# Optimization experiments

Hardware: AMD Instinct MI355X
Metric: run time of the kernel (lower is better)

Reference implementation:

```python
import jax, jax.numpy as jnp
import numpy as np

N_NODES = 100000
N_EDGES = 1600000
D_IN = 128
CH = [128, 128]
N_GRAPHS = 256


def _glorot(key, shape):
    lim = float(np.sqrt(6.0 / (shape[0] + shape[1])))
    return jax.random.uniform(key, shape, jnp.float32, -lim, lim)


def setup_inputs() -> dict:
    key = jax.random.key(0)
    ks = jax.random.split(key, 12)
    x = jax.random.normal(ks[0], (N_NODES, D_IN), jnp.float32)
    edge_index = jax.random.randint(ks[1], (2, N_EDGES), 0, N_NODES, jnp.int64)
    batch = jnp.sort(jax.random.randint(ks[2], (N_NODES,), 0, N_GRAPHS, jnp.int64))
    W1 = _glorot(ks[3], (D_IN, CH[0]))
    b1 = jnp.zeros((CH[0],), jnp.float32)
    W2 = _glorot(ks[4], (CH[0], CH[1]))
    b2 = jnp.zeros((CH[1],), jnp.float32)
    Wm1 = _glorot(ks[5], (CH[1], 500)); bm1 = jnp.zeros((500,), jnp.float32)
    Wm2 = _glorot(ks[6], (500, 100));   bm2 = jnp.zeros((100,), jnp.float32)
    Wm3 = _glorot(ks[7], (100, 1));     bm3 = jnp.zeros((1,), jnp.float32)
    return {"x": x, "edge_index": edge_index, "batch": batch,
            "W1": W1, "b1": b1, "W2": W2, "b2": b2,
            "Wm1": Wm1, "bm1": bm1, "Wm2": Wm2, "bm2": bm2,
            "Wm3": Wm3, "bm3": bm3}


def gcn_conv(x, W, b, src, dst, n_nodes):
    # GCNConv with add_self_loops=True, symmetric normalization.
    h = x @ W  # [N, C]
    deg = jnp.zeros((n_nodes,), h.dtype).at[dst].add(1.0) + 1.0  # +1 self loop
    dinv = jax.lax.rsqrt(deg)  # deg >= 1
    norm = dinv[src] * dinv[dst]  # [E]
    agg = jnp.zeros_like(h).at[dst].add(h[src] * norm[:, None])
    agg = agg + h * (dinv * dinv)[:, None]  # self-loop term, norm = dinv[i]^2
    return agg + b


def global_mean_pool(x, batch, n_graphs):
    s = jax.ops.segment_sum(x, batch, num_segments=n_graphs)
    cnt = jax.ops.segment_sum(jnp.ones((x.shape[0],), x.dtype), batch, num_segments=n_graphs)
    return s / jnp.maximum(cnt, 1.0)[:, None]


def reference(x, edge_index, batch, W1, b1, W2, b2, Wm1, bm1, Wm2, bm2, Wm3, bm3):
    src, dst = edge_index[0], edge_index[1]
    h = jax.nn.relu(gcn_conv(x, W1, b1, src, dst, N_NODES))
    h = jax.nn.relu(gcn_conv(h, W2, b2, src, dst, N_NODES))
    g = global_mean_pool(h, batch, N_GRAPHS)  # [G, CH1]
    g = jax.nn.relu(g @ Wm1 + bm1)
    g = jax.nn.relu(g @ Wm2 + bm2)
    return g @ Wm3 + bm3  # [G, 1]
```

## Files before the change

### kernel.cpp

```cpp
#include <hip/hip_runtime.h>

#define CDIM 128
#define NGRAPH 256
#define BSH 7
#define BCAP 4096
#define NBLK 256

typedef unsigned short bf16_t;
typedef __attribute__((ext_vector_type(8))) short bf16x8;
typedef __attribute__((ext_vector_type(4))) float f32x4;

__device__ __forceinline__ float bflo(unsigned u) { return __uint_as_float(u << 16); }
__device__ __forceinline__ float bfhi(unsigned u) { return __uint_as_float(u & 0xffff0000u); }
__device__ __forceinline__ unsigned short f2bf(float f) {
  unsigned u = __float_as_uint(f);
  u += 0x7fffu + ((u >> 16) & 1u);
  return (unsigned short)(u >> 16);
}

__global__ __launch_bounds__(1024) void k_phist(const int* __restrict__ dst,
    int* __restrict__ phist, const float* __restrict__ W1,
    const float* __restrict__ W2, bf16_t* __restrict__ Wtg1,
    bf16_t* __restrict__ Wtg2, float* __restrict__ gb, bf16_t* __restrict__ tz1,
    bf16_t* __restrict__ tz2, int N, int E, int NB) {
  __shared__ int hist[1024];
  int t = blockIdx.x, tid = threadIdx.x;
  int gidx = t * 1024 + tid;
  if (gidx < 16384) {
    int n = gidx >> 7, k = gidx & 127;
    Wtg1[n * 128 + k] = f2bf(W1[k * 128 + n]);
    Wtg2[n * 128 + k] = f2bf(W2[k * 128 + n]);
  }
  if (gidx < NGRAPH * CDIM) gb[gidx] = 0.f;
  if (gidx < 64) {
    ((unsigned*)(tz1 + (size_t)N * CDIM))[gidx] = 0u;
    ((unsigned*)(tz2 + (size_t)N * CDIM))[gidx] = 0u;
  }
  for (int i = tid; i < NB; i += 1024) hist[i] = 0;
  __syncthreads();
  int tile = (E + NBLK - 1) / NBLK;
  int lo = t * tile;
  int hi = lo + tile; if (hi > E) hi = E;
  for (int i = lo + tid; i < hi; i += 1024) atomicAdd(&hist[dst[i] >> BSH], 1);
  __syncthreads();
  for (int i = tid; i < NB; i += 1024) phist[i * NBLK + t] = hist[i];
}

__global__ __launch_bounds__(256) void k_bscan(int* __restrict__ phist,
    int* __restrict__ btot) {
  __shared__ int wsum[4];
  int b = blockIdx.x;
  int tid = threadIdx.x, lane = tid & 63, wave = tid >> 6;
  int orig = phist[b * NBLK + tid];
  int v = orig;
#pragma unroll
  for (int ofs = 1; ofs < 64; ofs <<= 1) {
    int u = __shfl_up(v, ofs, 64);
    if (lane >= ofs) v += u;
  }
  if (lane == 63) wsum[wave] = v;
  __syncthreads();
  int add = 0;
#pragma unroll
  for (int w = 0; w < 3; w++) if (w < wave) add += wsum[w];
  int incl = v + add;
  phist[b * NBLK + tid] = incl - orig;
  if (tid == 255) btot[b] = incl;
}

__global__ __launch_bounds__(1024) void k_pscatter(const int* __restrict__ src,
    const int* __restrict__ dst, const int* __restrict__ phist,
    const int* __restrict__ btot, unsigned* __restrict__ tmp, int E, int NB) {
  __shared__ int cur[1024];
  __shared__ int sh[1024];
  int t = blockIdx.x, tid = threadIdx.x;
  int v = (tid < NB) ? btot[tid] : 0;
  sh[tid] = v;
  __syncthreads();
  for (int ofs = 1; ofs < 1024; ofs <<= 1) {
    int u = (tid >= ofs) ? sh[tid - ofs] : 0;
    __syncthreads();
    sh[tid] += u;
    __syncthreads();
  }
  if (tid < NB) cur[tid] = (sh[tid] - v) + phist[tid * NBLK + t];
  __syncthreads();
  int tile = (E + NBLK - 1) / NBLK;
  int lo = t * tile;
  int hi = lo + tile; if (hi > E) hi = E;
  for (int i = lo + tid; i < hi; i += 1024) {
    int d = dst[i];
    int p = atomicAdd(&cur[d >> BSH], 1);
    tmp[p] = (unsigned)src[i] | ((unsigned)(d & 127) << 20);
  }
}

__global__ __launch_bounds__(256) void k_csort2(const unsigned* __restrict__ tmp,
    const int* __restrict__ btot, int* __restrict__ rowptr, float* __restrict__ dinv,
    int* __restrict__ col, int N, int NB, int E) {
  __shared__ int hist[128];
  __shared__ int sc[128];
  __shared__ int lcur[128];
  __shared__ int red[256];
  __shared__ unsigned buf[BCAP];
  int b = blockIdx.x;
  int n0 = b << BSH;
  int tid = threadIdx.x;
  int part = 0;
  for (int j = tid; j < b; j += 256) part += btot[j];
  red[tid] = part;
  __syncthreads();
  for (int ofs = 128; ofs > 0; ofs >>= 1) {
    if (tid < ofs) red[tid] += red[tid + ofs];
    __syncthreads();
  }
  int base = red[0];
  int cnt = btot[b];
  if (tid < 128) hist[tid] = 0;
  __syncthreads();
  for (int i = tid; i < cnt; i += 256) atomicAdd(&hist[(tmp[base + i] >> 20) & 127], 1);
  __syncthreads();
  if (tid < 128) sc[tid] = hist[tid];
  __syncthreads();
  for (int ofs = 1; ofs < 128; ofs <<= 1) {
    int v = (tid < 128 && tid >= ofs) ? sc[tid - ofs] : 0;
    __syncthreads();
    if (tid < 128) sc[tid] += v;
    __syncthreads();
  }
  if (tid < 128) {
    int excl = sc[tid] - hist[tid];
    lcur[tid] = excl;
    int node = n0 + tid;
    if (node < N) {
      rowptr[node] = base + excl;
      dinv[node] = rsqrtf((float)hist[tid] + 1.0f);
    }
  }
  if (b == 0 && tid == 0) rowptr[N] = E;
  __syncthreads();
  if (cnt <= BCAP) {
    for (int i = tid; i < cnt; i += 256) {
      unsigned pk = tmp[base + i];
      int p = atomicAdd(&lcur[(pk >> 20) & 127], 1);
      buf[p] = pk & 0xFFFFFu;
    }
    __syncthreads();
    for (int i = tid; i < cnt; i += 256) col[base + i] = (int)buf[i];
  } else {
    for (int i = tid; i < cnt; i += 256) {
      unsigned pk = tmp[base + i];
      int p = atomicAdd(&lcur[(pk >> 20) & 127], 1);
      col[base + p] = (int)(pk & 0xFFFFFu);
    }
  }
}

#define WSTRIDE 136
template <int BF16IN>
__global__ __launch_bounds__(256) void k_gemm(const void* __restrict__ Ap,
    const bf16_t* __restrict__ Wtg, const float* __restrict__ dscale,
    bf16_t* __restrict__ Co, int M) {
  __shared__ bf16_t Wt[128 * WSTRIDE];
  int tid = threadIdx.x;
  for (int c2 = tid; c2 < 2048; c2 += 256) {
    int n = c2 >> 4;
    int k8 = (c2 & 15) << 3;
    *(uint4*)&Wt[n * WSTRIDE + k8] = *(const uint4*)&Wtg[n * 128 + k8];
  }
  __syncthreads();

  int wave = tid >> 6;
  int lane = tid & 63;
  int m = lane & 15;
  int q = lane >> 4;
  int nstrips = (M + 63) >> 6;

  for (int s = blockIdx.x; s < nstrips; s += gridDim.x) {
    int rowA = s * 64 + wave * 16 + m;
    if (rowA > M - 1) rowA = M - 1;
    bf16x8 a[4];
#pragma unroll
    for (int c = 0; c < 4; c++) {
      if (BF16IN) {
        a[c] = *(const bf16x8*)((const bf16_t*)Ap + (size_t)rowA * CDIM + c * 32 + q * 8);
      } else {
        const float* ap = (const float*)Ap + (size_t)rowA * CDIM + c * 32 + q * 8;
        float4 f0 = *(const float4*)ap;
        float4 f1 = *(const float4*)(ap + 4);
        union { bf16x8 v; unsigned short u[8]; } ua;
        ua.u[0] = f2bf(f0.x); ua.u[1] = f2bf(f0.y); ua.u[2] = f2bf(f0.z); ua.u[3] = f2bf(f0.w);
        ua.u[4] = f2bf(f1.x); ua.u[5] = f2bf(f1.y); ua.u[6] = f2bf(f1.z); ua.u[7] = f2bf(f1.w);
        a[c] = ua.v;
      }
    }
    float sc[4];
#pragma unroll
    for (int r = 0; r < 4; r++) {
      int row = s * 64 + wave * 16 + q * 4 + r;
      sc[r] = (row < M) ? dscale[row] : 0.f;
    }
#pragma unroll
    for (int t = 0; t < 8; t++) {
      f32x4 acc = {0.f, 0.f, 0.f, 0.f};
#pragma unroll
      for (int c = 0; c < 4; c++) {
        bf16x8 bv = *(const bf16x8*)&Wt[(t * 16 + m) * WSTRIDE + c * 32 + q * 8];
        acc = __builtin_amdgcn_mfma_f32_16x16x32_bf16(a[c], bv, acc, 0, 0, 0);
      }
#pragma unroll
      for (int r = 0; r < 4; r++) {
        int row = s * 64 + wave * 16 + q * 4 + r;
        if (row < M) Co[(size_t)row * CDIM + t * 16 + m] = f2bf(acc[r] * sc[r]);
      }
    }
  }
}

#define GISS(S, V, JJ) \
  { _Pragma("unroll") for (int u = 0; u < 8; u++) \
      S[u] = __builtin_amdgcn_readlane(sL, (JJ) + u); \
    _Pragma("unroll") for (int u = 0; u < 8; u++) \
      V[u] = tp[(size_t)S[u] * 64 + lane]; }
#define GCON(V) \
  { _Pragma("unroll") for (int u = 0; u < 8; u++) { \
      a0 += bflo(V[u]); a1 += bfhi(V[u]); } }
#define GBLOCK(CNT) \
  { int nb = ((CNT) + 7) >> 3; \
    GISS(sA, vA, 0); \
    int b_ = 1; \
    for (; b_ + 1 < nb; b_ += 2) { \
      GISS(sB, vB, b_ * 8);       GCON(vA); \
      GISS(sA, vA, (b_ + 1) * 8); GCON(vB); \
    } \
    if (b_ < nb) { GISS(sB, vB, b_ * 8); GCON(vA); GCON(vB); } \
    else { GCON(vA); } }

__global__ __launch_bounds__(1024) void k_aggg(const bf16_t* __restrict__ t,
    const int* __restrict__ rowptr, const int* __restrict__ col,
    const float* __restrict__ dinv, const float* __restrict__ bias,
    const bf16_t* __restrict__ Wtg, bf16_t* __restrict__ to, int N) {
  __shared__ bf16_t Wt[128 * WSTRIDE];
  __shared__ unsigned hs[64 * 68];
  int tid = threadIdx.x;
  int wave = tid >> 6, lane = tid & 63;
  for (int c2 = tid; c2 < 2048; c2 += 1024) {
    int n = c2 >> 4, k8 = (c2 & 15) << 3;
    *(uint4*)&Wt[n * WSTRIDE + k8] = *(const uint4*)&Wtg[n * 128 + k8];
  }
  const unsigned* tp = (const unsigned*)t;
  float2 bb = ((const float2*)bias)[lane];
  int sA[8]; unsigned vA[8];
  int sB[8]; unsigned vB[8];
  int nbase = blockIdx.x * 64;
#pragma unroll 1
  for (int i = 0; i < 4; i++) {
    int node = nbase + wave * 4 + i;
    unsigned hv = 0u;
    if (node < N) {
      float di = dinv[node];
      unsigned sv = tp[(size_t)node * 64 + lane];
      float a0 = bflo(sv), a1 = bfhi(sv);
      int beg = rowptr[node], end = rowptr[node + 1];
      for (int base = beg; base < end; base += 64) {
        int cnt = end - base; if (cnt > 64) cnt = 64;
        int sL = N;
        if (lane < cnt) sL = col[base + lane];
        GBLOCK(cnt);
      }
      float o0 = fmaxf(fmaf(di, a0, bb.x), 0.f);
      float o1 = fmaxf(fmaf(di, a1, bb.y), 0.f);
      hv = ((unsigned)f2bf(o1) << 16) | f2bf(o0);
    }
    hs[(wave * 4 + i) * 68 + lane] = hv;
  }
  __syncthreads();
  int rg = wave & 3, cg = wave >> 2;
  int m = lane & 15, q = lane >> 4;
  bf16x8 a[4];
#pragma unroll
  for (int c = 0; c < 4; c++)
    a[c] = *(const bf16x8*)&hs[(rg * 16 + m) * 68 + c * 16 + q * 4];
  float sc4[4]; int rows[4];
#pragma unroll
  for (int r = 0; r < 4; r++) {
    int row = nbase + rg * 16 + q * 4 + r;
    rows[r] = row;
    sc4[r] = (row < N) ? dinv[row] : 0.f;
  }
#pragma unroll
  for (int tt = 0; tt < 2; tt++) {
    int tcol = cg * 2 + tt;
    f32x4 acc = {0.f, 0.f, 0.f, 0.f};
#pragma unroll
    for (int c = 0; c < 4; c++) {
      bf16x8 bv = *(const bf16x8*)&Wt[(tcol * 16 + m) * WSTRIDE + c * 32 + q * 8];
      acc = __builtin_amdgcn_mfma_f32_16x16x32_bf16(a[c], bv, acc, 0, 0, 0);
    }
#pragma unroll
    for (int r = 0; r < 4; r++)
      if (rows[r] < N)
        to[(size_t)rows[r] * CDIM + tcol * 16 + m] = f2bf(acc[r] * sc4[r]);
  }
}

__global__ __launch_bounds__(256) void k_aggp(const bf16_t* __restrict__ t,
    const int* __restrict__ rowptr, const int* __restrict__ col,
    const float* __restrict__ dinv, const float* __restrict__ bias,
    const int* __restrict__ batch, float* __restrict__ gsum, int N) {
  int wave = threadIdx.x >> 6;
  int lane = threadIdx.x & 63;
  int n0 = (blockIdx.x * 4 + wave) * 8;
  if (n0 >= N) return;
  int nEnd = n0 + 8; if (nEnd > N) nEnd = N;
  const unsigned* tp = (const unsigned*)t;
  float2 bb = ((const float2*)bias)[lane];
  float p0 = 0.f, p1 = 0.f;
  int curb = batch[n0];
  int sA[8]; unsigned vA[8];
  int sB[8]; unsigned vB[8];

  for (int node = n0; node < nEnd; node++) {
    float di = dinv[node];
    unsigned sv = tp[(size_t)node * 64 + lane];
    float a0 = bflo(sv);
    float a1 = bfhi(sv);
    int beg = rowptr[node], end = rowptr[node + 1];
    for (int base = beg; base < end; base += 64) {
      int cnt = end - base; if (cnt > 64) cnt = 64;
      int sL = N;
      if (lane < cnt) sL = col[base + lane];
      GBLOCK(cnt);
    }
    float o0 = fmaxf(fmaf(di, a0, bb.x), 0.f);
    float o1 = fmaxf(fmaf(di, a1, bb.y), 0.f);
    int b = batch[node];
    if (b != curb) {
      atomicAdd(&gsum[curb * CDIM + 2 * lane], p0);
      atomicAdd(&gsum[curb * CDIM + 2 * lane + 1], p1);
      curb = b; p0 = p1 = 0.f;
    }
    p0 += __uint_as_float((unsigned)f2bf(o0) << 16);
    p1 += __uint_as_float((unsigned)f2bf(o1) << 16);
  }
  atomicAdd(&gsum[curb * CDIM + 2 * lane], p0);
  atomicAdd(&gsum[curb * CDIM + 2 * lane + 1], p1);
}

__global__ __launch_bounds__(512) void k_mlp(const float* __restrict__ g,
    const int* __restrict__ batch, int N,
    const float* __restrict__ Wm1, const float* __restrict__ bm1,
    const float* __restrict__ Wm2, const float* __restrict__ bm2,
    const float* __restrict__ wm3, const float* __restrict__ bm3,
    float* __restrict__ out) {
  __shared__ float gs[CDIM];
  __shared__ float m1s[500];
  __shared__ float m2s[100];
  int bi = blockIdx.x, tid = threadIdx.x;
  if (tid < CDIM) {
    int lo = 0, hi = N;
    while (lo < hi) { int mid = (lo + hi) >> 1; if (batch[mid] < bi) lo = mid + 1; else hi = mid; }
    int s = lo;
    lo = 0; hi = N;
    int key = bi + 1;
    while (lo < hi) { int mid = (lo + hi) >> 1; if (batch[mid] < key) lo = mid + 1; else hi = mid; }
    float inv = 1.f / fmaxf((float)(lo - s), 1.f);
    gs[tid] = g[bi * CDIM + tid] * inv;
  }
  __syncthreads();
  if (tid < 500) {
    float acc = bm1[tid];
#pragma unroll 4
    for (int k = 0; k < CDIM; k++) acc = fmaf(gs[k], Wm1[k * 500 + tid], acc);
    m1s[tid] = fmaxf(acc, 0.f);
  }
  __syncthreads();
  if (tid < 100) {
    float acc = bm2[tid];
    for (int k = 0; k < 500; k++) acc = fmaf(m1s[k], Wm2[k * 100 + tid], acc);
    m2s[tid] = fmaxf(acc, 0.f) * wm3[tid];
  }
  __syncthreads();
  if (tid < 64) {
    float v = m2s[tid] + ((tid + 64 < 100) ? m2s[tid + 64] : 0.f);
#pragma unroll
    for (int ofs = 32; ofs > 0; ofs >>= 1) v += __shfl_down(v, ofs, 64);
    if (tid == 0) out[bi] = v + bm3[0];
  }
}

static inline size_t align_up(size_t v) { return (v + 255) & ~(size_t)255; }

extern "C" void kernel_launch(void* const* d_in, const int* in_sizes, int n_in,
                              void* d_out, int out_size, void* d_ws, size_t ws_size,
                              hipStream_t stream) {
  const float* x   = (const float*)d_in[0];
  const int*   ei  = (const int*)d_in[1];
  const int*   bat = (const int*)d_in[2];
  const float* W1  = (const float*)d_in[3];
  const float* b1  = (const float*)d_in[4];
  const float* W2  = (const float*)d_in[5];
  const float* b2  = (const float*)d_in[6];
  const float* Wm1 = (const float*)d_in[7];
  const float* bm1 = (const float*)d_in[8];
  const float* Wm2 = (const float*)d_in[9];
  const float* bm2 = (const float*)d_in[10];
  const float* Wm3 = (const float*)d_in[11];
  const float* bm3 = (const float*)d_in[12];
  float* out = (float*)d_out;

  const int E = in_sizes[1] / 2;
  const int N = in_sizes[2];
  const int* src = ei;
  const int* dst = ei + E;
  const int NB = (N + 127) >> BSH;
  const int M  = NB * NBLK;

  char* p = (char*)d_ws;
  bf16_t* t    = (bf16_t*)p;   p += align_up((size_t)(N + 1) * CDIM * 2);
  bf16_t* t2   = (bf16_t*)p;   p += align_up((size_t)(N + 1) * CDIM * 2);
  int* rowptr  = (int*)p;      p += align_up((size_t)(N + 1) * 4);
  int* colx    = (int*)p;      p += align_up((size_t)E * 4);
  unsigned* tmp= (unsigned*)p; p += align_up((size_t)E * 4);
  float* dinv  = (float*)p;    p += align_up((size_t)N * 4);
  int* phist   = (int*)p;      p += align_up((size_t)M * 4);
  int* btot    = (int*)p;      p += align_up((size_t)NB * 4);
  bf16_t* Wtg1 = (bf16_t*)p;   p += align_up((size_t)CDIM * CDIM * 2);
  bf16_t* Wtg2 = (bf16_t*)p;   p += align_up((size_t)CDIM * CDIM * 2);
  float* gb    = (float*)p;    p += align_up((size_t)NGRAPH * CDIM * 4);
  (void)ws_size; (void)n_in; (void)out_size;

  k_phist<<<NBLK, 1024, 0, stream>>>(dst, phist, W1, W2, Wtg1, Wtg2, gb, t, t2, N, E, NB);
  k_bscan<<<NB, 256, 0, stream>>>(phist, btot);
  k_pscatter<<<NBLK, 1024, 0, stream>>>(src, dst, phist, btot, tmp, E, NB);
  k_csort2<<<NB, 256, 0, stream>>>(tmp, btot, rowptr, dinv, colx, N, NB, E);

  k_gemm<0><<<512, 256, 0, stream>>>(x, Wtg1, dinv, t, N);
  k_aggg<<<(N + 63) / 64, 1024, 0, stream>>>(t, rowptr, colx, dinv, b1, Wtg2, t2, N);
  int pw = (N + 7) / 8;
  k_aggp<<<(pw + 3) / 4, 256, 0, stream>>>(t2, rowptr, colx, dinv, b2, bat, gb, N);
  k_mlp<<<NGRAPH, 512, 0, stream>>>(gb, bat, N, Wm1, bm1, Wm2, bm2, Wm3, bm3, out);
}
```

Measured before the change: 327.6 us.

## Stage scatter tile in LDS for coalesced writes; retune aggp and gemm grids

The partition scatter kernel now builds a local bucket histogram and prefix sum per tile, stages each tile's packed edges in shared memory sorted by bucket, then writes them out contiguously per bucket. This replaces random global writes with mostly contiguous runs. Separately, the pooling aggregation gives each wave 16 nodes instead of 8, and the first GEMM launches twice as many blocks. The LDS staging uses about 43KB of shared memory and extra scans and barriers per block.

```diff
diff --git a/kernel.cpp b/kernel.cpp
--- a/kernel.cpp
+++ b/kernel.cpp
@@ -5,6 +5,7 @@
 #define BSH 7
 #define BCAP 4096
 #define NBLK 256
+#define TILE 6272
 
 typedef unsigned short bf16_t;
 typedef __attribute__((ext_vector_type(8))) short bf16x8;
@@ -71,27 +72,62 @@
 __global__ __launch_bounds__(1024) void k_pscatter(const int* __restrict__ src,
     const int* __restrict__ dst, const int* __restrict__ phist,
     const int* __restrict__ btot, unsigned* __restrict__ tmp, int E, int NB) {
-  __shared__ int cur[1024];
-  __shared__ int sh[1024];
+  __shared__ int lh[1024];
+  __shared__ int ls[1024];
+  __shared__ int lc[1024];
+  __shared__ int gb2[1024];
+  __shared__ unsigned short sbkt[TILE];
+  __shared__ unsigned sbuf[TILE];
   int t = blockIdx.x, tid = threadIdx.x;
+
   int v = (tid < NB) ? btot[tid] : 0;
-  sh[tid] = v;
+  ls[tid] = v;
   __syncthreads();
   for (int ofs = 1; ofs < 1024; ofs <<= 1) {
-    int u = (tid >= ofs) ? sh[tid - ofs] : 0;
-    __syncthreads();
-    sh[tid] += u;
-    __syncthreads();
-  }
-  if (tid < NB) cur[tid] = (sh[tid] - v) + phist[tid * NBLK + t];
-  __syncthreads();
+    int u = (tid >= ofs) ? ls[tid - ofs] : 0;
+    __syncthreads();
+    ls[tid] += u;
+    __syncthreads();
+  }
+  if (tid < NB) gb2[tid] = (ls[tid] - v) + phist[tid * NBLK + t];
+  lh[tid] = 0;
+  __syncthreads();
+
   int tile = (E + NBLK - 1) / NBLK;
   int lo = t * tile;
   int hi = lo + tile; if (hi > E) hi = E;
-  for (int i = lo + tid; i < hi; i += 1024) {
-    int d = dst[i];
-    int p = atomicAdd(&cur[d >> BSH], 1);
-    tmp[p] = (unsigned)src[i] | ((unsigned)(d & 127) << 20);
+  int cnt = hi - lo;
+
+  for (int i = tid; i < cnt; i += 1024) atomicAdd(&lh[dst[lo + i] >> BSH], 1);
+  __syncthreads();
+  int h = lh[tid];
+  ls[tid] = h;
+  __syncthreads();
+  for (int ofs = 1; ofs < 1024; ofs <<= 1) {
+    int u = (tid >= ofs) ? ls[tid - ofs] : 0;
+    __syncthreads();
+    ls[tid] += u;
+    __syncthreads();
+  }
+  int excl = ls[tid] - h;
+  __syncthreads();
+  ls[tid] = excl;
+  lc[tid] = excl;
+  __syncthreads();
+
+  for (int i = tid; i < cnt; i += 1024) {
+    int d = dst[lo + i];
+    int b = d >> BSH;
+    unsigned pk = (unsigned)src[lo + i] | ((unsigned)(d & 127) << 20);
+    int p = atomicAdd(&lc[b], 1);
+    sbuf[p] = pk;
+    sbkt[p] = (unsigned short)b;
+  }
+  __syncthreads();
+
+  for (int j = tid; j < cnt; j += 1024) {
+    int b = sbkt[j];
+    tmp[gb2[b] + (j - ls[b])] = sbuf[j];
   }
 }
 
@@ -310,9 +346,9 @@
     const int* __restrict__ batch, float* __restrict__ gsum, int N) {
   int wave = threadIdx.x >> 6;
   int lane = threadIdx.x & 63;
-  int n0 = (blockIdx.x * 4 + wave) * 8;
+  int n0 = (blockIdx.x * 4 + wave) * 16;
   if (n0 >= N) return;
-  int nEnd = n0 + 8; if (nEnd > N) nEnd = N;
+  int nEnd = n0 + 16; if (nEnd > N) nEnd = N;
   const unsigned* tp = (const unsigned*)t;
   float2 bb = ((const float2*)bias)[lane];
   float p0 = 0.f, p1 = 0.f;
@@ -435,9 +471,9 @@
   k_pscatter<<<NBLK, 1024, 0, stream>>>(src, dst, phist, btot, tmp, E, NB);
   k_csort2<<<NB, 256, 0, stream>>>(tmp, btot, rowptr, dinv, colx, N, NB, E);
 
-  k_gemm<0><<<512, 256, 0, stream>>>(x, Wtg1, dinv, t, N);
+  k_gemm<0><<<1024, 256, 0, stream>>>(x, Wtg1, dinv, t, N);
   k_aggg<<<(N + 63) / 64, 1024, 0, stream>>>(t, rowptr, colx, dinv, b1, Wtg2, t2, N);
-  int pw = (N + 7) / 8;
-  k_aggp<<<(pw + 3) / 4, 256, 0, stream>>>(t2, rowptr, colx, dinv, b2, bat, gb, N);
+  int pwaves = (N + 15) / 16;
+  k_aggp<<<(pwaves + 3) / 4, 256, 0, stream>>>(t2, rowptr, colx, dinv, b2, bat, gb, N);
   k_mlp<<<NGRAPH, 512, 0, stream>>>(gb, bat, N, Wm1, bm1, Wm2, bm2, Wm3, bm3, out);
 }
```

New measurement: 316.8 us, median of 2. 1.03x faster.
